# Performance work log

Measured on AMD Instinct MI355X. Metric: run time of the kernel, lower is better.

The kernel has to match this reference:

```python
import jax, jax.numpy as jnp
import numpy as np

N_EMBD = 2048
NUM_GROUPS = 8
EXPERTS_PER_GROUP = 8
ROUTER_TEMPERATURE = 1.0
N_TOKENS = 16384


def setup_inputs() -> dict:
    key = jax.random.key(0)
    kx, kg, ke = jax.random.split(key, 3)
    x = jax.random.normal(kx, (N_TOKENS, N_EMBD), dtype=jnp.float32)
    # nn.Linear(in, out, bias=False) stores weight as [out, in]; kaiming-uniform-ish scale
    bound = 1.0 / np.sqrt(N_EMBD)
    group_gate_w = jax.random.uniform(kg, (NUM_GROUPS, N_EMBD), dtype=jnp.float32,
                                      minval=-bound, maxval=bound)
    expert_gate_w = jax.random.uniform(ke, (NUM_GROUPS * EXPERTS_PER_GROUP, N_EMBD),
                                       dtype=jnp.float32, minval=-bound, maxval=bound)
    return {"x": x, "group_gate_w": group_gate_w, "expert_gate_w": expert_gate_w}


def reference(x, group_gate_w, expert_gate_w):
    N = x.shape[0]
    G = NUM_GROUPS
    E_g = EXPERTS_PER_GROUP
    inv_temp = 1.0 / ROUTER_TEMPERATURE

    # Level 1: group routing
    group_logits = jnp.einsum('nd,gd->ng', x, group_gate_w)            # [N, G]
    group_probs = jax.nn.softmax(group_logits * inv_temp, axis=-1)     # [N, G]
    group_mask = group_probs >= (1.0 / G)                              # [N, G]

    # Level 2: expert routing within each group
    expert_logits = jnp.einsum('nd,ed->ne', x, expert_gate_w)          # [N, G*E_g]
    expert_logits = expert_logits.reshape(N, G, E_g)
    expert_probs = jax.nn.softmax(expert_logits * inv_temp, axis=-1)   # [N, G, E_g]
    expert_mask = expert_probs >= (1.0 / E_g)                          # [N, G, E_g]

    valid_mask_3d = group_mask[:, :, None] & expert_mask               # [N, G, E_g]
    selected_weights_3d = (group_probs[:, :, None] * expert_probs) * valid_mask_3d.astype(x.dtype)

    valid_mask = valid_mask_3d.reshape(N, G * E_g)
    selected_weights = selected_weights_3d.reshape(N, G * E_g)
    weight_sum = jnp.clip(jnp.sum(selected_weights, axis=-1, keepdims=True), 1e-9, None)
    normalized_weights = selected_weights / weight_sum
    return (valid_mask, normalized_weights)
```

## Files before the change

### kernel.cpp

```cpp
#include <hip/hip_runtime.h>


#define NT 16384
#define NE 2048
#define NTH 512
#define NBLK 256
#define NCHUNK 32
#define WCH 20480
#define XCH 16384
#define XOFF 40960
#define LDS_BYTES 76800

typedef _Float16 v8h __attribute__((ext_vector_type(8)));
typedef float    v4f __attribute__((ext_vector_type(4)));

__global__ __launch_bounds__(256, 1)
void prep(const float* __restrict__ gw, const float* __restrict__ ew,
          _Float16* __restrict__ wf)
{
    const int t = blockIdx.x * 256 + threadIdx.x;
    const int j    = t & 7;
    const int sl   = (t >> 3) & 63;
    const int rest = t >> 9;
    const int g    = rest % 5;
    const int ks   = rest / 5;
    const int m = sl & 15, q = sl >> 4;
    const int gate = g * 16 + m;
    const int k = ks * 32 + q * 8 + j;
    float v = 0.f;
    if (gate < 64)      v = ew[gate * NE + k];
    else if (gate < 72) v = gw[(gate - 64) * NE + k];
    const _Float16 h = (_Float16)v;
    const int o = (((ks * 5 + g) * 2) * 64 + sl) * 8 + j;
    wf[o]       = h;
    wf[o + 512] = (_Float16)((v - (float)h) * 2048.0f);
}

__global__ __launch_bounds__(NTH, 2)
void router(const float* __restrict__ x, const _Float16* __restrict__ wf,
            float* __restrict__ out)
{
    __shared__ __align__(16) char sm[LDS_BYTES];
    const int tid  = threadIdx.x;
    const int lane = tid & 63;
    const int w    = tid >> 6;
    const int tt   = w >> 1, s2 = w & 1;
    const int t0   = blockIdx.x * 64;

    const int xtok = tid >> 3, xks = tid & 7;
    const float* xsrc = x + (size_t)(t0 + xtok) * NE + xks * 8;
    const int xa16 = (((xtok >> 4) * 2 + (xks >> 2)) * 2) * 64
                   + (((xks & 3) * 16 + (xtok & 15)) ^ xks);

    uint4 wr0, wr1, wr2;

    auto wload = [&](int c) {
        const char* src = (const char*)wf + (size_t)c * WCH;
        wr0 = *(const uint4*)(src + (0 * 512 + tid) * 16);
        wr1 = *(const uint4*)(src + (1 * 512 + tid) * 16);
        if (tid < 256) wr2 = *(const uint4*)(src + (1024 + tid) * 16);
    };
    auto wcommit = [&](int buf) {
        char* dst = sm + buf * WCH;
        *(uint4*)(dst + (0 * 512 + tid) * 16) = wr0;
        *(uint4*)(dst + (1 * 512 + tid) * 16) = wr1;
        if (tid < 256) *(uint4*)(dst + (1024 + tid) * 16) = wr2;
    };
    auto xload_to = [&](int c, float4& r0, float4& r1) {
        const float* p = xsrc + c * 64;
        r0 = *(const float4*)(p);
        r1 = *(const float4*)(p + 4);
    };
    auto xcommit_from = [&](const float4& a, const float4& b, int buf) {
        const float v[8] = {a.x, a.y, a.z, a.w, b.x, b.y, b.z, b.w};
        v8h h, l;
        #pragma unroll
        for (int j = 0; j < 8; ++j) {
            const _Float16 hh = (_Float16)v[j];
            h[j] = hh;
            l[j] = (_Float16)((v[j] - (float)hh) * 2048.0f);
        }
        char* xb = sm + XOFF + buf * XCH;
        *(v8h*)(xb + xa16 * 16)        = h;
        *(v8h*)(xb + (xa16 + 64) * 16) = l;
    };

    v4f accH[5], accC[5];
    #pragma unroll
    for (int g = 0; g < 5; ++g) { accH[g] = (v4f)(0.f); accC[g] = (v4f)(0.f); }

    const int xrd = (((tt * 2 + s2) * 2) * 64 + (lane ^ (s2 * 4 + (lane >> 4)))) * 16;
    const int wrd = ((s2 * 5) * 2) * 1024 + lane * 16;

    auto compute = [&](int P) {
        const char* xb = sm + XOFF + P * XCH;
        const char* wb = sm + P * WCH;
        const v8h Bh = *(const v8h*)(xb + xrd);
        const v8h Bl = *(const v8h*)(xb + xrd + 1024);
        #pragma unroll
        for (int g = 0; g < 5; ++g) {
            const char* wpg = wb + wrd + g * 2048;
            const v8h Ah = *(const v8h*)(wpg);
            const v8h Al = *(const v8h*)(wpg + 1024);
            accH[g] = __builtin_amdgcn_mfma_f32_16x16x32_f16(Ah, Bh, accH[g], 0, 0, 0);
            accC[g] = __builtin_amdgcn_mfma_f32_16x16x32_f16(Ah, Bl, accC[g], 0, 0, 0);
            accC[g] = __builtin_amdgcn_mfma_f32_16x16x32_f16(Al, Bh, accC[g], 0, 0, 0);
        }
    };

    float4 xA0, xA1, xB0, xB1;

    wload(0);
    xload_to(0, xA0, xA1);
    wcommit(0);
    xcommit_from(xA0, xA1, 0);
    xload_to(1, xB0, xB1);

    auto step = [&](int c, int P, float4& cur0, float4& cur1,
                    const float4& prv0, const float4& prv1) {
        __syncthreads();
        if (c + 1 < NCHUNK) wload(c + 1);
        if (c + 2 < NCHUNK) xload_to(c + 2, cur0, cur1);
        compute(P);
        if (c + 1 < NCHUNK) { wcommit(1 - P); xcommit_from(prv0, prv1, 1 - P); }
    };

    #pragma unroll 1
    for (int cc = 0; cc < NCHUNK; cc += 2) {
        step(cc,     0, xA0, xA1, xB0, xB1);
        step(cc + 1, 1, xB0, xB1, xA0, xA1);
    }
    __syncthreads();

    float part[5][4];
    #pragma unroll
    for (int g = 0; g < 5; ++g)
        #pragma unroll
        for (int r = 0; r < 4; ++r)
            part[g][r] = accH[g][r] + accC[g][r] * (1.0f / 2048.0f);

    float* red = (float*)sm;
    if (s2 == 1) {
        #pragma unroll
        for (int g = 0; g < 5; ++g)
            #pragma unroll
            for (int r = 0; r < 4; ++r)
                red[((tt * 5 + g) * 4 + r) * 64 + lane] = part[g][r];
    }
    __syncthreads();
    float* la = (float*)(sm + 20480);
    if (s2 == 0) {
        #pragma unroll
        for (int g = 0; g < 5; ++g)
            #pragma unroll
            for (int r = 0; r < 4; ++r) {
                const float v = part[g][r] + red[((tt * 5 + g) * 4 + r) * 64 + lane];
                const int gate  = g * 16 + (lane >> 4) * 4 + r;
                const int token = tt * 16 + (lane & 15);
                la[token * 84 + gate] = v;
            }
    }
    __syncthreads();

    if (lane < 8) {
        const int token = w * 8 + lane;
        const float* lg = la + token * 84;
        float* M  = (float*)(sm + 41984) + token * 64;
        float* Wn = (float*)(sm + 58368) + token * 64;

        float gpb[8];
        float gmax = lg[64];
        #pragma unroll
        for (int g = 1; g < 8; ++g) gmax = fmaxf(gmax, lg[64 + g]);
        float gsum = 0.f;
        #pragma unroll
        for (int g = 0; g < 8; ++g) { gpb[g] = __expf(lg[64 + g] - gmax); gsum += gpb[g]; }
        const float ginv = 1.f / gsum;

        float sel[64];
        float wsum = 0.f;
        #pragma unroll
        for (int g = 0; g < 8; ++g) {
            const float gp_ = gpb[g] * ginv;
            float emax = lg[g * 8];
            #pragma unroll
            for (int j = 1; j < 8; ++j) emax = fmaxf(emax, lg[g * 8 + j]);
            float ep[8]; float esum = 0.f;
            #pragma unroll
            for (int j = 0; j < 8; ++j) { ep[j] = __expf(lg[g * 8 + j] - emax); esum += ep[j]; }
            const float einv = 1.f / esum;
            const bool gm = gp_ >= 0.125f;
            #pragma unroll
            for (int j = 0; j < 8; ++j) {
                const float pe = ep[j] * einv;
                const bool v = gm && (pe >= 0.125f);
                const float ww = v ? gp_ * pe : 0.f;
                M[g * 8 + j] = v ? 1.f : 0.f;
                sel[g * 8 + j] = ww;
                wsum += ww;
            }
        }
        const float inv = 1.f / fmaxf(wsum, 1e-9f);
        #pragma unroll
        for (int e = 0; e < 64; ++e) Wn[e] = sel[e] * inv;
    }
    __syncthreads();

    const float4* M4 = (const float4*)(sm + 41984);
    const float4* W4 = (const float4*)(sm + 58368);
    float4* o0 = (float4*)(out + (size_t)t0 * 64);
    float4* o1 = (float4*)(out + (size_t)NT * 64 + (size_t)t0 * 64);
    o0[tid]       = M4[tid];
    o0[tid + 512] = M4[tid + 512];
    o1[tid]       = W4[tid];
    o1[tid + 512] = W4[tid + 512];
}

extern "C" void kernel_launch(void* const* d_in, const int* in_sizes, int n_in,
                              void* d_out, int out_size, void* d_ws, size_t ws_size,
                              hipStream_t stream) {
    const float* x  = (const float*)d_in[0];
    const float* gw = (const float*)d_in[1];
    const float* ew = (const float*)d_in[2];
    float* out = (float*)d_out;
    _Float16* wf = (_Float16*)d_ws;
    (void)ws_size; (void)in_sizes; (void)n_in; (void)out_size;

    prep<<<dim3(640), dim3(256), 0, stream>>>(gw, ew, wf);
    router<<<dim3(NBLK), dim3(NTH), 0, stream>>>(x, wf, out);
}
```

Baseline: 209.3 us.

## Load x directly into MFMA B-operand registers, bypassing LDS staging

Each lane now loads its own x fragment straight from global memory in the layout the MFMA B operand needs, then does the fp16 hi/lo split in registers. The x double-buffer in LDS, with its swizzled write and read, is removed. This cuts LDS traffic and per-chunk store/load work, and it shrinks LDS use. The cost is that global x reads are now strided per lane (16 tokens by 32-byte pieces), which may coalesce worse.

Result: no change. 210.9 us (+0.7%).

```diff
diff --git a/kernel.cpp b/kernel.cpp
--- a/kernel.cpp
+++ b/kernel.cpp
@@ -7,9 +7,7 @@
 #define NBLK 256
 #define NCHUNK 32
 #define WCH 20480
-#define XCH 16384
-#define XOFF 40960
-#define LDS_BYTES 76800
+#define LDS_BYTES 74752
 
 typedef _Float16 v8h __attribute__((ext_vector_type(8)));
 typedef float    v4f __attribute__((ext_vector_type(4)));
@@ -47,13 +45,10 @@
     const int tt   = w >> 1, s2 = w & 1;
     const int t0   = blockIdx.x * 64;
 
-    const int xtok = tid >> 3, xks = tid & 7;
-    const float* xsrc = x + (size_t)(t0 + xtok) * NE + xks * 8;
-    const int xa16 = (((xtok >> 4) * 2 + (xks >> 2)) * 2) * 64
-                   + (((xks & 3) * 16 + (xtok & 15)) ^ xks);
+    const float* xq = x + (size_t)(t0 + tt * 16 + (lane & 15)) * NE
+                    + s2 * 32 + (lane >> 4) * 8;
 
     uint4 wr0, wr1, wr2;
-
     auto wload = [&](int c) {
         const char* src = (const char*)wf + (size_t)c * WCH;
         wr0 = *(const uint4*)(src + (0 * 512 + tid) * 16);
@@ -66,37 +61,21 @@
         *(uint4*)(dst + (1 * 512 + tid) * 16) = wr1;
         if (tid < 256) *(uint4*)(dst + (1024 + tid) * 16) = wr2;
     };
-    auto xload_to = [&](int c, float4& r0, float4& r1) {
-        const float* p = xsrc + c * 64;
-        r0 = *(const float4*)(p);
-        r1 = *(const float4*)(p + 4);
-    };
-    auto xcommit_from = [&](const float4& a, const float4& b, int buf) {
-        const float v[8] = {a.x, a.y, a.z, a.w, b.x, b.y, b.z, b.w};
-        v8h h, l;
-        #pragma unroll
-        for (int j = 0; j < 8; ++j) {
-            const _Float16 hh = (_Float16)v[j];
-            h[j] = hh;
-            l[j] = (_Float16)((v[j] - (float)hh) * 2048.0f);
-        }
-        char* xb = sm + XOFF + buf * XCH;
-        *(v8h*)(xb + xa16 * 16)        = h;
-        *(v8h*)(xb + (xa16 + 64) * 16) = l;
-    };
 
     v4f accH[5], accC[5];
     #pragma unroll
     for (int g = 0; g < 5; ++g) { accH[g] = (v4f)(0.f); accC[g] = (v4f)(0.f); }
 
-    const int xrd = (((tt * 2 + s2) * 2) * 64 + (lane ^ (s2 * 4 + (lane >> 4)))) * 16;
-    const int wrd = ((s2 * 5) * 2) * 1024 + lane * 16;
-
-    auto compute = [&](int P) {
-        const char* xb = sm + XOFF + P * XCH;
+    const int wrd = s2 * 10240 + lane * 16;
+
+    auto xload_to = [&](int c, float4& r0, float4& r1) {
+        const float* p = xq + c * 64;
+        r0 = *(const float4*)(p);
+        r1 = *(const float4*)(p + 4);
+    };
+
+    auto mfma_block = [&](int P, const v8h& Bh, const v8h& Bl) {
         const char* wb = sm + P * WCH;
-        const v8h Bh = *(const v8h*)(xb + xrd);
-        const v8h Bl = *(const v8h*)(xb + xrd + 1024);
         #pragma unroll
         for (int g = 0; g < 5; ++g) {
             const char* wpg = wb + wrd + g * 2048;
@@ -108,27 +87,36 @@
         }
     };
 
+    auto step = [&](int c, int P, float4& cur0, float4& cur1) {
+        __syncthreads();
+        if (c + 1 < NCHUNK) wload(c + 1);
+        v8h Bh, Bl;
+        {
+            const float v[8] = {cur0.x, cur0.y, cur0.z, cur0.w,
+                                cur1.x, cur1.y, cur1.z, cur1.w};
+            #pragma unroll
+            for (int j = 0; j < 8; ++j) {
+                const _Float16 hh = (_Float16)v[j];
+                Bh[j] = hh;
+                Bl[j] = (_Float16)((v[j] - (float)hh) * 2048.0f);
+            }
+        }
+        if (c + 2 < NCHUNK) xload_to(c + 2, cur0, cur1);
+        mfma_block(P, Bh, Bl);
+        if (c + 1 < NCHUNK) wcommit(1 - P);
+    };
+
     float4 xA0, xA1, xB0, xB1;
 
     wload(0);
     xload_to(0, xA0, xA1);
+    xload_to(1, xB0, xB1);
     wcommit(0);
-    xcommit_from(xA0, xA1, 0);
-    xload_to(1, xB0, xB1);
-
-    auto step = [&](int c, int P, float4& cur0, float4& cur1,
-                    const float4& prv0, const float4& prv1) {
-        __syncthreads();
-        if (c + 1 < NCHUNK) wload(c + 1);
-        if (c + 2 < NCHUNK) xload_to(c + 2, cur0, cur1);
-        compute(P);
-        if (c + 1 < NCHUNK) { wcommit(1 - P); xcommit_from(prv0, prv1, 1 - P); }
-    };
 
     #pragma unroll 1
     for (int cc = 0; cc < NCHUNK; cc += 2) {
-        step(cc,     0, xA0, xA1, xB0, xB1);
-        step(cc + 1, 1, xB0, xB1, xA0, xA1);
+        step(cc,     0, xA0, xA1);
+        step(cc + 1, 1, xB0, xB1);
     }
     __syncthreads();
 
```
